# Kernel optimization log

Hardware: AMD Instinct MI355X
Metric: run time of the kernel (lower is better)

## Reference

```python
import jax, jax.numpy as jnp
import numpy as np

BN_EPS = 1e-5
N_LAYERS = 3


def _mlp_bn(h, w1, b1, g, beta, w2, b2):
    # Linear -> BatchNorm1d (batch stats, training-mode math) -> ReLU -> Linear
    h = h @ w1 + b1
    mu = jnp.mean(h, axis=0)
    var = jnp.var(h, axis=0)
    h = (h - mu) * jax.lax.rsqrt(var + BN_EPS) * g + beta
    h = jax.nn.relu(h)
    return h @ w2 + b2


def setup_inputs() -> dict:
    key = jax.random.key(0)
    ks = jax.random.split(key, 20)
    N, E, XD, ED, H, C, G = 50000, 640000, 64, 16, 128, 10, 512
    L = N_LAYERS
    s = lambda fan: 1.0 / np.sqrt(fan)
    inp = {
        "x": jax.random.normal(ks[0], (N, XD), jnp.float32),
        "edge_attr": jax.random.normal(ks[1], (E, ED), jnp.float32),
        "node_w": jax.random.uniform(ks[2], (XD, H), jnp.float32, -s(XD), s(XD)),
        "node_b": jnp.zeros((H,), jnp.float32),
        "edge_w": jax.random.uniform(ks[3], (ED, H), jnp.float32, -s(ED), s(ED)),
        "edge_b": jnp.zeros((H,), jnp.float32),
        "lin1_w": jax.random.uniform(ks[4], (L, H, H), jnp.float32, -s(H), s(H)),
        "lin1_b": jnp.zeros((L, H), jnp.float32),
        "bn_g": jnp.ones((L, H), jnp.float32),
        "bn_b": jnp.zeros((L, H), jnp.float32),
        "lin2_w": jax.random.uniform(ks[5], (L, H, H), jnp.float32, -s(H), s(H)),
        "lin2_b": jnp.zeros((L, H), jnp.float32),
        "fc_w": jax.random.uniform(ks[6], (H, C), jnp.float32, -s(H), s(H)),
        "fc_b": jnp.zeros((C,), jnp.float32),
        "edge_index": jax.random.randint(ks[7], (2, E), 0, N, jnp.int64),
        "batch": jnp.sort(jax.random.randint(ks[8], (N,), 0, G, jnp.int64)),
        "num_graphs": G,
    }
    return inp


def reference(x, edge_attr, node_w, node_b, edge_w, edge_b, lin1_w, lin1_b,
              bn_g, bn_b, lin2_w, lin2_b, fc_w, fc_b, edge_index, batch, num_graphs):
    N = x.shape[0]
    src, dst = edge_index[0], edge_index[1]
    h = x @ node_w + node_b                      # [N, H] node encoder
    e = edge_attr @ edge_w + edge_b              # [E, H] edge encoder
    for i in range(N_LAYERS):
        # GINEConv: msg = relu(h[src] + e); aggr = segment_sum at dst; out = MLP(h + aggr) (eps=0)
        msg = jax.nn.relu(h[src] + e)            # [E, H]
        aggr = jax.ops.segment_sum(msg, dst, num_segments=N)
        h = _mlp_bn(h + aggr, lin1_w[i], lin1_b[i], bn_g[i], bn_b[i], lin2_w[i], lin2_b[i])
        h = jax.nn.relu(h)                       # dropout p=0 -> identity
    pooled = jax.ops.segment_sum(h, batch, num_segments=num_graphs)  # global_add_pool
    return pooled @ fc_w + fc_b
```

## Files before the change

### kernel.cpp

```cpp
#include <hip/hip_runtime.h>

#define H   128

typedef __attribute__((ext_vector_type(8))) short short8;
typedef __attribute__((ext_vector_type(4))) float f32x4;

__device__ __forceinline__ unsigned int bfr(float f) {
  unsigned int u = __float_as_uint(f);
  return (u + 0x7fffu + ((u >> 16) & 1u)) >> 16;
}
__device__ __forceinline__ float bf_lo(unsigned int d) {
  return __uint_as_float(d << 16);
}
__device__ __forceinline__ float bf_hi(unsigned int d) {
  return __uint_as_float(d & 0xffff0000u);
}

__global__ __launch_bounds__(128) void node_enc(const float* __restrict__ x,
    const float* __restrict__ w, const float* __restrict__ b,
    unsigned int* __restrict__ h2, int N) {
  int row = blockIdx.x;
  if (row >= N) return;
  int j = threadIdx.x;
  __shared__ float xs[64];
  if (j < 64) xs[j] = x[(size_t)row * 64 + j];
  __syncthreads();
  float acc = b[j];
#pragma unroll
  for (int k = 0; k < 64; ++k) acc = fmaf(xs[k], w[k * H + j], acc);
  float part = __shfl_down(acc, 1, 64);
  if ((j & 1) == 0) {
    unsigned int d = bfr(acc) | (bfr(part) << 16);
    h2[(size_t)row * 64 + (j >> 1)] = d;
  }
}

__global__ __launch_bounds__(256) void count_deg(const int* __restrict__ dst,
    int* __restrict__ cnt, int E) {
  int e = blockIdx.x * 256 + threadIdx.x;
  if (e < E) atomicAdd(&cnt[dst[e]], 1);
}

__global__ __launch_bounds__(256) void block_sum(const int* __restrict__ cnt,
    int* __restrict__ bsum, int N) {
  int t = threadIdx.x;
  int i = blockIdx.x * 256 + t;
  int v = (i < N) ? cnt[i] : 0;
#pragma unroll
  for (int o = 32; o > 0; o >>= 1) v += __shfl_down(v, o, 64);
  __shared__ int wt[4];
  if ((t & 63) == 0) wt[t >> 6] = v;
  __syncthreads();
  if (t == 0) bsum[blockIdx.x] = wt[0] + wt[1] + wt[2] + wt[3];
}

__global__ __launch_bounds__(1024) void scan_bsum(const int* __restrict__ bsum,
    int* __restrict__ bbase, int nb) {
  __shared__ int s[1024];
  int t = threadIdx.x;
  int v = (t < nb) ? bsum[t] : 0;
  s[t] = v;
  __syncthreads();
  for (int o = 1; o < 1024; o <<= 1) {
    int u = (t >= o) ? s[t - o] : 0;
    __syncthreads();
    s[t] += u;
    __syncthreads();
  }
  if (t < nb) bbase[t] = s[t] - v;
}

__global__ __launch_bounds__(256) void scan_pass(const int* __restrict__ cnt,
    const int* __restrict__ bbase, int* __restrict__ off,
    int* __restrict__ cursor, int N) {
  int t = threadIdx.x;
  int i = blockIdx.x * 256 + t;
  int v = (i < N) ? cnt[i] : 0;
  int lane = t & 63;
  int incl = v;
#pragma unroll
  for (int o = 1; o < 64; o <<= 1) {
    int u = __shfl_up(incl, o, 64);
    if (lane >= o) incl += u;
  }
  __shared__ int wtot[4];
  int w = t >> 6;
  if (lane == 63) wtot[w] = incl;
  __syncthreads();
  if (t == 0) {
    int run = 0;
#pragma unroll
    for (int k = 0; k < 4; ++k) { int tmp = wtot[k]; wtot[k] = run; run += tmp; }
  }
  __syncthreads();
  int excl = incl - v + wtot[w] + bbase[blockIdx.x];
  if (i < N) { off[i] = excl; cursor[i] = excl; }
  if (i == N - 1) off[N] = excl + v;
}

__global__ __launch_bounds__(256) void scatter_csr(const int* __restrict__ src,
    const int* __restrict__ dst, int* __restrict__ cursor,
    int* __restrict__ perm, int* __restrict__ src_perm, int E) {
  int e = blockIdx.x * 256 + threadIdx.x;
  if (e < E) {
    int pos = atomicAdd(&cursor[dst[e]], 1);
    perm[pos] = e;
    src_perm[pos] = src[e];
  }
}

__global__ __launch_bounds__(256) void wpack(const float* __restrict__ w1,
    const float* __restrict__ w2, unsigned short* __restrict__ wp, int L) {
  int idx = blockIdx.x * 256 + threadIdx.x;
  int total = L * 2 * 16384;
  if (idx >= total) return;
  int j    = idx & 7;
  int lane = (idx >> 3) & 63;
  int ct   = (idx >> 9) & 7;
  int kt   = (idx >> 12) & 3;
  int mat  = idx >> 14;
  int l = mat >> 1, which = mat & 1;
  const float* w = (which == 0 ? w1 : w2) + (size_t)l * H * H;
  int k = kt * 32 + (lane >> 4) * 8 + j;
  int n = ct * 16 + (lane & 15);
  wp[idx] = (unsigned short)bfr(w[k * H + n]);
}

__global__ __launch_bounds__(256) void aggr_csr(const float* __restrict__ ea,
    const float* __restrict__ ew, const float* __restrict__ eb,
    const int* __restrict__ perm, const int* __restrict__ src_perm,
    const int* __restrict__ off, const unsigned int* __restrict__ h2,
    unsigned int* __restrict__ zb, int N) {
  int wid = threadIdx.x >> 6, lane = threadIdx.x & 63;
  int n = blockIdx.x * 4 + wid;
  if (n >= N) return;
  int beg = off[n], end = off[n + 1];
  int c = lane * 2;
  float2 wc[16];
#pragma unroll
  for (int k = 0; k < 16; ++k) wc[k] = *(const float2*)&ew[k * H + c];
  float2 bias = *(const float2*)&eb[c];
  float ax = 0.f, ay = 0.f;
  int i = beg;
  for (; i + 2 <= end; i += 2) {
    int e0 = __builtin_amdgcn_readfirstlane(perm[i]);
    int e1 = __builtin_amdgcn_readfirstlane(perm[i + 1]);
    int s0 = __builtin_amdgcn_readfirstlane(src_perm[i]);
    int s1 = __builtin_amdgcn_readfirstlane(src_perm[i + 1]);
    unsigned int hv0 = h2[(size_t)s0 * 64 + lane];
    unsigned int hv1 = h2[(size_t)s1 * 64 + lane];
    const float* a0 = ea + (size_t)e0 * 16;
    const float* a1 = ea + (size_t)e1 * 16;
    float x0 = bias.x, y0 = bias.y, x1 = bias.x, y1 = bias.y;
#pragma unroll
    for (int k = 0; k < 16; ++k) {
      float a0k = a0[k], a1k = a1[k];
      x0 = fmaf(a0k, wc[k].x, x0);
      y0 = fmaf(a0k, wc[k].y, y0);
      x1 = fmaf(a1k, wc[k].x, x1);
      y1 = fmaf(a1k, wc[k].y, y1);
    }
    ax += fmaxf(x0 + bf_lo(hv0), 0.f) + fmaxf(x1 + bf_lo(hv1), 0.f);
    ay += fmaxf(y0 + bf_hi(hv0), 0.f) + fmaxf(y1 + bf_hi(hv1), 0.f);
  }
  if (i < end) {
    int e0 = __builtin_amdgcn_readfirstlane(perm[i]);
    int s0 = __builtin_amdgcn_readfirstlane(src_perm[i]);
    unsigned int hv0 = h2[(size_t)s0 * 64 + lane];
    const float* a0 = ea + (size_t)e0 * 16;
    float x0 = bias.x, y0 = bias.y;
#pragma unroll
    for (int k = 0; k < 16; ++k) {
      float a0k = a0[k];
      x0 = fmaf(a0k, wc[k].x, x0);
      y0 = fmaf(a0k, wc[k].y, y0);
    }
    ax += fmaxf(x0 + bf_lo(hv0), 0.f);
    ay += fmaxf(y0 + bf_hi(hv0), 0.f);
  }
  unsigned int hn = h2[(size_t)n * 64 + lane];
  float zx = bf_lo(hn) + ax, zy = bf_hi(hn) + ay;
  zb[(size_t)n * 64 + lane] = bfr(zx) | (bfr(zy) << 16);
}

__global__ __launch_bounds__(256) void mlp1m(const unsigned short* __restrict__ zb,
    const unsigned short* __restrict__ wp, const float* __restrict__ b1,
    float* __restrict__ tout, float* __restrict__ sum,
    float* __restrict__ sumsq, int N) {
  int tid = threadIdx.x;
  int wave = tid >> 6, lane = tid & 63;
  int q = lane >> 4, m = lane & 15;
  int r0 = blockIdx.x * 64 + wave * 16;
  f32x4 acc[8];
#pragma unroll
  for (int ct = 0; ct < 8; ++ct) acc[ct] = (f32x4){0.f, 0.f, 0.f, 0.f};
#pragma unroll
  for (int kt = 0; kt < 4; ++kt) {
    short8 a = *(const short8*)(zb + (size_t)(r0 + m) * H + kt * 32 + q * 8);
#pragma unroll
    for (int ct = 0; ct < 8; ++ct) {
      short8 b = *(const short8*)(wp + ((size_t)(kt * 8 + ct) * 64 + lane) * 8);
      acc[ct] = __builtin_amdgcn_mfma_f32_16x16x32_bf16(a, b, acc[ct], 0, 0, 0);
    }
  }
  __shared__ float red[2][H][16];
  int wq = wave * 4 + q;
#pragma unroll
  for (int ct = 0; ct < 8; ++ct) {
    int col = ct * 16 + m;
    float bias = b1[col];
    float s1 = 0.f, s2 = 0.f;
#pragma unroll
    for (int r = 0; r < 4; ++r) {
      int gr = r0 + q * 4 + r;
      float v = acc[ct][r] + bias;
      if (gr < N) {
        tout[(size_t)gr * H + col] = v;
        s1 += v;
        s2 += v * v;
      }
    }
    red[0][col][wq] = s1;
    red[1][col][wq] = s2;
  }
  __syncthreads();
  if (tid < H) {
    float a = 0.f, b = 0.f;
#pragma unroll
    for (int g = 0; g < 16; ++g) {
      a += red[0][tid][g];
      b += red[1][tid][g];
    }
    atomicAdd(&sum[tid], a);
    atomicAdd(&sumsq[tid], b);
  }
}

__global__ void bn_finalize(const float* __restrict__ sum,
    const float* __restrict__ sumsq, const float* __restrict__ g,
    const float* __restrict__ beta, float* __restrict__ scale,
    float* __restrict__ shift, float invN) {
  int j = threadIdx.x;
  float mu = sum[j] * invN;
  float var = sumsq[j] * invN - mu * mu;
  float inv = rsqrtf(var + 1e-5f);
  float sc = g[j] * inv;
  scale[j] = sc;
  shift[j] = beta[j] - mu * sc;
}

__global__ __launch_bounds__(256) void mlp2m(const float* __restrict__ tin,
    const float* __restrict__ scale, const float* __restrict__ shift,
    const unsigned short* __restrict__ wp, const float* __restrict__ b2,
    unsigned short* __restrict__ hout, int N,
    const int* __restrict__ batch, float* __restrict__ pooled) {
  int tid = threadIdx.x;
  int wave = tid >> 6, lane = tid & 63;
  int q = lane >> 4, m = lane & 15;
  int r0 = blockIdx.x * 64 + wave * 16;
  f32x4 acc[8];
#pragma unroll
  for (int ct = 0; ct < 8; ++ct) acc[ct] = (f32x4){0.f, 0.f, 0.f, 0.f};
#pragma unroll
  for (int kt = 0; kt < 4; ++kt) {
    int col0 = kt * 32 + q * 8;
    f32x4 t0 = *(const f32x4*)(tin + (size_t)(r0 + m) * H + col0);
    f32x4 t1 = *(const f32x4*)(tin + (size_t)(r0 + m) * H + col0 + 4);
    f32x4 sc0 = *(const f32x4*)(scale + col0);
    f32x4 sc1 = *(const f32x4*)(scale + col0 + 4);
    f32x4 sh0 = *(const f32x4*)(shift + col0);
    f32x4 sh1 = *(const f32x4*)(shift + col0 + 4);
    short8 a;
#pragma unroll
    for (int j = 0; j < 4; ++j) {
      float v = fmaxf(fmaf(t0[j], sc0[j], sh0[j]), 0.f);
      a[j] = (short)bfr(v);
    }
#pragma unroll
    for (int j = 0; j < 4; ++j) {
      float v = fmaxf(fmaf(t1[j], sc1[j], sh1[j]), 0.f);
      a[4 + j] = (short)bfr(v);
    }
#pragma unroll
    for (int ct = 0; ct < 8; ++ct) {
      short8 b = *(const short8*)(wp + ((size_t)(kt * 8 + ct) * 64 + lane) * 8);
      acc[ct] = __builtin_amdgcn_mfma_f32_16x16x32_bf16(a, b, acc[ct], 0, 0, 0);
    }
  }
#pragma unroll
  for (int ct = 0; ct < 8; ++ct) {
    float bias = b2[ct * 16 + m];
#pragma unroll
    for (int r = 0; r < 4; ++r) acc[ct][r] = fmaxf(acc[ct][r] + bias, 0.f);
  }
  if (hout != nullptr) {
#pragma unroll
    for (int r = 0; r < 4; ++r) {
      int gr = r0 + q * 4 + r;
      if (gr < N) {
#pragma unroll
        for (int ct = 0; ct < 8; ++ct)
          hout[(size_t)gr * H + ct * 16 + m] = (unsigned short)bfr(acc[ct][r]);
      }
    }
  }
  if (pooled != nullptr) {
    int bprev = -1;
    float pa[8];
#pragma unroll
    for (int ct = 0; ct < 8; ++ct) pa[ct] = 0.f;
    for (int r = 0; r < 4; ++r) {
      int gr = r0 + q * 4 + r;
      if (gr >= N) break;
      int bb = batch[gr];
      if (bb != bprev && bprev >= 0) {
#pragma unroll
        for (int ct = 0; ct < 8; ++ct) {
          atomicAdd(&pooled[(size_t)bprev * H + ct * 16 + m], pa[ct]);
          pa[ct] = 0.f;
        }
      }
      bprev = bb;
#pragma unroll
      for (int ct = 0; ct < 8; ++ct) pa[ct] += acc[ct][r];
    }
    if (bprev >= 0) {
#pragma unroll
      for (int ct = 0; ct < 8; ++ct)
        atomicAdd(&pooled[(size_t)bprev * H + ct * 16 + m], pa[ct]);
    }
  }
}

__global__ __launch_bounds__(128) void fc_kernel(const float* __restrict__ pooled,
    const float* __restrict__ w, const float* __restrict__ b,
    float* __restrict__ out, int C) {
  int g = blockIdx.x;
  int j = threadIdx.x;
  __shared__ float p[H];
  p[j] = pooled[(size_t)g * H + j];
  __syncthreads();
  if (j < C) {
    float acc = b[j];
#pragma unroll 4
    for (int k = 0; k < H; ++k) acc = fmaf(p[k], w[k * C + j], acc);
    out[(size_t)g * C + j] = acc;
  }
}

extern "C" void kernel_launch(void* const* d_in, const int* in_sizes, int n_in,
                              void* d_out, int out_size, void* d_ws, size_t ws_size,
                              hipStream_t stream) {
  const float* x         = (const float*)d_in[0];
  const float* edge_attr = (const float*)d_in[1];
  const float* node_w    = (const float*)d_in[2];
  const float* node_b    = (const float*)d_in[3];
  const float* edge_w    = (const float*)d_in[4];
  const float* edge_b    = (const float*)d_in[5];
  const float* lin1_w    = (const float*)d_in[6];
  const float* lin1_b    = (const float*)d_in[7];
  const float* bn_g      = (const float*)d_in[8];
  const float* bn_b      = (const float*)d_in[9];
  const float* lin2_w    = (const float*)d_in[10];
  const float* lin2_b    = (const float*)d_in[11];
  const float* fc_w      = (const float*)d_in[12];
  const float* fc_b      = (const float*)d_in[13];
  const int*   edge_index= (const int*)d_in[14];
  const int*   batch     = (const int*)d_in[15];

  int N = in_sizes[0] / 64;
  int E = in_sizes[1] / 16;
  int C = in_sizes[13];
  int G = out_size / C;

  const int* src = edge_index;
  const int* dst = edge_index + E;

  int mblk = (N + 63) / 64;
  int Npad = mblk * 64;

  float* t      = (float*)d_ws;
  float* pooled = t + (size_t)Npad * H;
  float* sums   = pooled + (size_t)G * H;
  float* sumsq  = sums + H;
  float* scale  = sumsq + H;
  float* shift  = scale + H;
  unsigned int* h2 = (unsigned int*)(shift + H);
  unsigned int* zb = h2 + (size_t)Npad * 64;
  unsigned short* wp = (unsigned short*)(zb + (size_t)Npad * 64);
  int* cnt      = (int*)(wp + 6 * 16384);
  int* off      = cnt + N;
  int* cursor   = off + N + 1;
  int* src_perm = cursor + N;
  int* perm     = src_perm + E;
  int* bsum     = perm + E;
  int* bbase    = bsum + 1024;

  int nb = (N + 255) / 256;

  hipMemsetAsync(cnt, 0, (size_t)N * sizeof(int), stream);
  count_deg<<<(E + 255) / 256, 256, 0, stream>>>(dst, cnt, E);
  block_sum<<<nb, 256, 0, stream>>>(cnt, bsum, N);
  scan_bsum<<<1, 1024, 0, stream>>>(bsum, bbase, nb);
  scan_pass<<<nb, 256, 0, stream>>>(cnt, bbase, off, cursor, N);
  scatter_csr<<<(E + 255) / 256, 256, 0, stream>>>(src, dst, cursor, perm, src_perm, E);
  wpack<<<(6 * 16384 + 255) / 256, 256, 0, stream>>>(lin1_w, lin2_w, wp, 3);

  node_enc<<<N, 128, 0, stream>>>(x, node_w, node_b, h2, N);

  int ablk = (N + 3) / 4;
  for (int l = 0; l < 3; ++l) {
    hipMemsetAsync(sums, 0, 2 * H * sizeof(float), stream);
    aggr_csr<<<ablk, 256, 0, stream>>>(edge_attr, edge_w, edge_b, perm,
                                       src_perm, off, h2, zb, N);
    mlp1m<<<mblk, 256, 0, stream>>>((const unsigned short*)zb,
                                    wp + (size_t)(l * 2 + 0) * 16384,
                                    lin1_b + (size_t)l * H, t, sums, sumsq, N);
    bn_finalize<<<1, H, 0, stream>>>(sums, sumsq, bn_g + (size_t)l * H,
                                     bn_b + (size_t)l * H, scale, shift, 1.0f / N);
    bool last = (l == 2);
    if (last) hipMemsetAsync(pooled, 0, (size_t)G * H * sizeof(float), stream);
    mlp2m<<<mblk, 256, 0, stream>>>(t, scale, shift,
                                    wp + (size_t)(l * 2 + 1) * 16384,
                                    lin2_b + (size_t)l * H,
                                    last ? nullptr : (unsigned short*)h2, N,
                                    batch, last ? pooled : nullptr);
  }

  fc_kernel<<<G, 128, 0, stream>>>(pooled, fc_w, fc_b, (float*)d_out, C);
}
```

Before: 629.8 us.

## Balance edge aggregation with fixed-size edge chunks and boundary atomics

Replaces the per-node CSR aggregation, where each wave handled one destination node, with an edge-balanced scheme. Each wave now takes a fixed-size chunk of dst-sorted edges and flushes partial sums with float atomics into an fp32 z buffer whenever the destination changes. The h+aggr addition and bf16 conversion move into mlp1m. bn_finalize is folded into the prologue of mlp2m, and the BN stat buffers are zeroed once up front. The intent is to remove load imbalance from variable node degrees and drop launches, at the cost of a per-layer memset of an N×H fp32 buffer, more atomics, and doubled z traffic in fp32.

After: 646.7 us. 2.7% more time.

```diff
diff --git a/kernel.cpp b/kernel.cpp
--- a/kernel.cpp
+++ b/kernel.cpp
@@ -100,12 +100,15 @@
 
 __global__ __launch_bounds__(256) void scatter_csr(const int* __restrict__ src,
     const int* __restrict__ dst, int* __restrict__ cursor,
-    int* __restrict__ perm, int* __restrict__ src_perm, int E) {
+    int* __restrict__ perm, int* __restrict__ src_perm,
+    int* __restrict__ dst_perm, int E) {
   int e = blockIdx.x * 256 + threadIdx.x;
   if (e < E) {
-    int pos = atomicAdd(&cursor[dst[e]], 1);
+    int d = dst[e];
+    int pos = atomicAdd(&cursor[d], 1);
     perm[pos] = e;
     src_perm[pos] = src[e];
+    dst_perm[pos] = d;
   }
 }
 
@@ -126,27 +129,31 @@
   wp[idx] = (unsigned short)bfr(w[k * H + n]);
 }
 
-__global__ __launch_bounds__(256) void aggr_csr(const float* __restrict__ ea,
+__global__ __launch_bounds__(256) void aggr_chunk(const float* __restrict__ ea,
     const float* __restrict__ ew, const float* __restrict__ eb,
     const int* __restrict__ perm, const int* __restrict__ src_perm,
-    const int* __restrict__ off, const unsigned int* __restrict__ h2,
-    unsigned int* __restrict__ zb, int N) {
-  int wid = threadIdx.x >> 6, lane = threadIdx.x & 63;
-  int n = blockIdx.x * 4 + wid;
-  if (n >= N) return;
-  int beg = off[n], end = off[n + 1];
+    const int* __restrict__ dst_perm, const unsigned int* __restrict__ h2,
+    float* __restrict__ z, int E, int CH) {
+  int wv = blockIdx.x * 4 + (threadIdx.x >> 6);
+  int lane = threadIdx.x & 63;
+  int i0 = wv * CH;
+  int i1 = min(E, i0 + CH);
+  if (i0 >= i1) return;
   int c = lane * 2;
   float2 wc[16];
 #pragma unroll
   for (int k = 0; k < 16; ++k) wc[k] = *(const float2*)&ew[k * H + c];
   float2 bias = *(const float2*)&eb[c];
+  int cur = __builtin_amdgcn_readfirstlane(dst_perm[i0]);
   float ax = 0.f, ay = 0.f;
-  int i = beg;
-  for (; i + 2 <= end; i += 2) {
+  int i = i0;
+  for (; i + 2 <= i1; i += 2) {
     int e0 = __builtin_amdgcn_readfirstlane(perm[i]);
     int e1 = __builtin_amdgcn_readfirstlane(perm[i + 1]);
     int s0 = __builtin_amdgcn_readfirstlane(src_perm[i]);
     int s1 = __builtin_amdgcn_readfirstlane(src_perm[i + 1]);
+    int d0 = __builtin_amdgcn_readfirstlane(dst_perm[i]);
+    int d1 = __builtin_amdgcn_readfirstlane(dst_perm[i + 1]);
     unsigned int hv0 = h2[(size_t)s0 * 64 + lane];
     unsigned int hv1 = h2[(size_t)s1 * 64 + lane];
     const float* a0 = ea + (size_t)e0 * 16;
@@ -160,12 +167,27 @@
       x1 = fmaf(a1k, wc[k].x, x1);
       y1 = fmaf(a1k, wc[k].y, y1);
     }
-    ax += fmaxf(x0 + bf_lo(hv0), 0.f) + fmaxf(x1 + bf_lo(hv1), 0.f);
-    ay += fmaxf(y0 + bf_hi(hv0), 0.f) + fmaxf(y1 + bf_hi(hv1), 0.f);
-  }
-  if (i < end) {
+    if (d0 != cur) {
+      atomicAdd(&z[(size_t)cur * H + c], ax);
+      atomicAdd(&z[(size_t)cur * H + c + 1], ay);
+      ax = ay = 0.f;
+      cur = d0;
+    }
+    ax += fmaxf(x0 + bf_lo(hv0), 0.f);
+    ay += fmaxf(y0 + bf_hi(hv0), 0.f);
+    if (d1 != cur) {
+      atomicAdd(&z[(size_t)cur * H + c], ax);
+      atomicAdd(&z[(size_t)cur * H + c + 1], ay);
+      ax = ay = 0.f;
+      cur = d1;
+    }
+    ax += fmaxf(x1 + bf_lo(hv1), 0.f);
+    ay += fmaxf(y1 + bf_hi(hv1), 0.f);
+  }
+  if (i < i1) {
     int e0 = __builtin_amdgcn_readfirstlane(perm[i]);
     int s0 = __builtin_amdgcn_readfirstlane(src_perm[i]);
+    int d0 = __builtin_amdgcn_readfirstlane(dst_perm[i]);
     unsigned int hv0 = h2[(size_t)s0 * 64 + lane];
     const float* a0 = ea + (size_t)e0 * 16;
     float x0 = bias.x, y0 = bias.y;
@@ -175,28 +197,46 @@
       x0 = fmaf(a0k, wc[k].x, x0);
       y0 = fmaf(a0k, wc[k].y, y0);
     }
+    if (d0 != cur) {
+      atomicAdd(&z[(size_t)cur * H + c], ax);
+      atomicAdd(&z[(size_t)cur * H + c + 1], ay);
+      ax = ay = 0.f;
+      cur = d0;
+    }
     ax += fmaxf(x0 + bf_lo(hv0), 0.f);
     ay += fmaxf(y0 + bf_hi(hv0), 0.f);
   }
-  unsigned int hn = h2[(size_t)n * 64 + lane];
-  float zx = bf_lo(hn) + ax, zy = bf_hi(hn) + ay;
-  zb[(size_t)n * 64 + lane] = bfr(zx) | (bfr(zy) << 16);
-}
-
-__global__ __launch_bounds__(256) void mlp1m(const unsigned short* __restrict__ zb,
-    const unsigned short* __restrict__ wp, const float* __restrict__ b1,
-    float* __restrict__ tout, float* __restrict__ sum,
-    float* __restrict__ sumsq, int N) {
+  atomicAdd(&z[(size_t)cur * H + c], ax);
+  atomicAdd(&z[(size_t)cur * H + c + 1], ay);
+}
+
+__global__ __launch_bounds__(256) void mlp1m(const float* __restrict__ z,
+    const unsigned int* __restrict__ h2, const unsigned short* __restrict__ wp,
+    const float* __restrict__ b1, float* __restrict__ tout,
+    float* __restrict__ sum, float* __restrict__ sumsq, int N) {
   int tid = threadIdx.x;
   int wave = tid >> 6, lane = tid & 63;
   int q = lane >> 4, m = lane & 15;
   int r0 = blockIdx.x * 64 + wave * 16;
+  int row = r0 + m;
   f32x4 acc[8];
 #pragma unroll
   for (int ct = 0; ct < 8; ++ct) acc[ct] = (f32x4){0.f, 0.f, 0.f, 0.f};
 #pragma unroll
   for (int kt = 0; kt < 4; ++kt) {
-    short8 a = *(const short8*)(zb + (size_t)(r0 + m) * H + kt * 32 + q * 8);
+    int c0 = kt * 32 + q * 8;
+    f32x4 z0 = *(const f32x4*)(z + (size_t)row * H + c0);
+    f32x4 z1 = *(const f32x4*)(z + (size_t)row * H + c0 + 4);
+    uint4 hh = *(const uint4*)(h2 + (size_t)row * 64 + (c0 >> 1));
+    short8 a;
+    a[0] = (short)bfr(z0[0] + bf_lo(hh.x));
+    a[1] = (short)bfr(z0[1] + bf_hi(hh.x));
+    a[2] = (short)bfr(z0[2] + bf_lo(hh.y));
+    a[3] = (short)bfr(z0[3] + bf_hi(hh.y));
+    a[4] = (short)bfr(z1[0] + bf_lo(hh.z));
+    a[5] = (short)bfr(z1[1] + bf_hi(hh.z));
+    a[6] = (short)bfr(z1[2] + bf_lo(hh.w));
+    a[7] = (short)bfr(z1[3] + bf_hi(hh.w));
 #pragma unroll
     for (int ct = 0; ct < 8; ++ct) {
       short8 b = *(const short8*)(wp + ((size_t)(kt * 8 + ct) * 64 + lane) * 8);
@@ -236,49 +276,44 @@
   }
 }
 
-__global__ void bn_finalize(const float* __restrict__ sum,
-    const float* __restrict__ sumsq, const float* __restrict__ g,
-    const float* __restrict__ beta, float* __restrict__ scale,
-    float* __restrict__ shift, float invN) {
-  int j = threadIdx.x;
-  float mu = sum[j] * invN;
-  float var = sumsq[j] * invN - mu * mu;
-  float inv = rsqrtf(var + 1e-5f);
-  float sc = g[j] * inv;
-  scale[j] = sc;
-  shift[j] = beta[j] - mu * sc;
-}
-
 __global__ __launch_bounds__(256) void mlp2m(const float* __restrict__ tin,
-    const float* __restrict__ scale, const float* __restrict__ shift,
+    const float* __restrict__ sums, const float* __restrict__ sumsqs,
+    const float* __restrict__ bng, const float* __restrict__ bnb,
     const unsigned short* __restrict__ wp, const float* __restrict__ b2,
-    unsigned short* __restrict__ hout, int N,
+    unsigned short* __restrict__ hout, int N, float invN,
     const int* __restrict__ batch, float* __restrict__ pooled) {
   int tid = threadIdx.x;
+  __shared__ float scs[H], shs[H];
+  if (tid < H) {
+    float mu = sums[tid] * invN;
+    float var = sumsqs[tid] * invN - mu * mu;
+    float inv = rsqrtf(var + 1e-5f);
+    float sc = bng[tid] * inv;
+    scs[tid] = sc;
+    shs[tid] = bnb[tid] - mu * sc;
+  }
+  __syncthreads();
   int wave = tid >> 6, lane = tid & 63;
   int q = lane >> 4, m = lane & 15;
   int r0 = blockIdx.x * 64 + wave * 16;
+  int row = r0 + m;
   f32x4 acc[8];
 #pragma unroll
   for (int ct = 0; ct < 8; ++ct) acc[ct] = (f32x4){0.f, 0.f, 0.f, 0.f};
 #pragma unroll
   for (int kt = 0; kt < 4; ++kt) {
-    int col0 = kt * 32 + q * 8;
-    f32x4 t0 = *(const f32x4*)(tin + (size_t)(r0 + m) * H + col0);
-    f32x4 t1 = *(const f32x4*)(tin + (size_t)(r0 + m) * H + col0 + 4);
-    f32x4 sc0 = *(const f32x4*)(scale + col0);
-    f32x4 sc1 = *(const f32x4*)(scale + col0 + 4);
-    f32x4 sh0 = *(const f32x4*)(shift + col0);
-    f32x4 sh1 = *(const f32x4*)(shift + col0 + 4);
+    int c0 = kt * 32 + q * 8;
+    f32x4 t0 = *(const f32x4*)(tin + (size_t)row * H + c0);
+    f32x4 t1 = *(const f32x4*)(tin + (size_t)row * H + c0 + 4);
     short8 a;
 #pragma unroll
     for (int j = 0; j < 4; ++j) {
-      float v = fmaxf(fmaf(t0[j], sc0[j], sh0[j]), 0.f);
+      float v = fmaxf(fmaf(t0[j], scs[c0 + j], shs[c0 + j]), 0.f);
       a[j] = (short)bfr(v);
     }
 #pragma unroll
     for (int j = 0; j < 4; ++j) {
-      float v = fmaxf(fmaf(t1[j], sc1[j], sh1[j]), 0.f);
+      float v = fmaxf(fmaf(t1[j], scs[c0 + 4 + j], shs[c0 + 4 + j]), 0.f);
       a[4 + j] = (short)bfr(v);
     }
 #pragma unroll
@@ -380,19 +415,17 @@
   int Npad = mblk * 64;
 
   float* t      = (float*)d_ws;
-  float* pooled = t + (size_t)Npad * H;
-  float* sums   = pooled + (size_t)G * H;
-  float* sumsq  = sums + H;
-  float* scale  = sumsq + H;
-  float* shift  = scale + H;
-  unsigned int* h2 = (unsigned int*)(shift + H);
-  unsigned int* zb = h2 + (size_t)Npad * 64;
-  unsigned short* wp = (unsigned short*)(zb + (size_t)Npad * 64);
+  float* z      = t + (size_t)Npad * H;
+  float* pooled = z + (size_t)Npad * H;
+  float* sumsA  = pooled + (size_t)G * H;
+  unsigned int* h2 = (unsigned int*)(sumsA + 3 * 256);
+  unsigned short* wp = (unsigned short*)(h2 + (size_t)Npad * 64);
   int* cnt      = (int*)(wp + 6 * 16384);
   int* off      = cnt + N;
   int* cursor   = off + N + 1;
   int* src_perm = cursor + N;
-  int* perm     = src_perm + E;
+  int* dst_perm = src_perm + E;
+  int* perm     = dst_perm + E;
   int* bsum     = perm + E;
   int* bbase    = bsum + 1024;
 
@@ -403,28 +436,32 @@
   block_sum<<<nb, 256, 0, stream>>>(cnt, bsum, N);
   scan_bsum<<<1, 1024, 0, stream>>>(bsum, bbase, nb);
   scan_pass<<<nb, 256, 0, stream>>>(cnt, bbase, off, cursor, N);
-  scatter_csr<<<(E + 255) / 256, 256, 0, stream>>>(src, dst, cursor, perm, src_perm, E);
+  scatter_csr<<<(E + 255) / 256, 256, 0, stream>>>(src, dst, cursor, perm,
+                                                   src_perm, dst_perm, E);
   wpack<<<(6 * 16384 + 255) / 256, 256, 0, stream>>>(lin1_w, lin2_w, wp, 3);
+  hipMemsetAsync(sumsA, 0, 3 * 256 * sizeof(float), stream);
 
   node_enc<<<N, 128, 0, stream>>>(x, node_w, node_b, h2, N);
 
-  int ablk = (N + 3) / 4;
+  const int NWAVE = 8192;
+  int CH = (E + NWAVE - 1) / NWAVE;
+  int ablk = ( (E + CH - 1) / CH + 3 ) / 4;
+
   for (int l = 0; l < 3; ++l) {
-    hipMemsetAsync(sums, 0, 2 * H * sizeof(float), stream);
-    aggr_csr<<<ablk, 256, 0, stream>>>(edge_attr, edge_w, edge_b, perm,
-                                       src_perm, off, h2, zb, N);
-    mlp1m<<<mblk, 256, 0, stream>>>((const unsigned short*)zb,
-                                    wp + (size_t)(l * 2 + 0) * 16384,
-                                    lin1_b + (size_t)l * H, t, sums, sumsq, N);
-    bn_finalize<<<1, H, 0, stream>>>(sums, sumsq, bn_g + (size_t)l * H,
-                                     bn_b + (size_t)l * H, scale, shift, 1.0f / N);
+    hipMemsetAsync(z, 0, (size_t)N * H * sizeof(float), stream);
+    aggr_chunk<<<ablk, 256, 0, stream>>>(edge_attr, edge_w, edge_b, perm,
+                                         src_perm, dst_perm, h2, z, E, CH);
+    mlp1m<<<mblk, 256, 0, stream>>>(z, h2, wp + (size_t)(l * 2 + 0) * 16384,
+                                    lin1_b + (size_t)l * H, t,
+                                    sumsA + l * 256, sumsA + l * 256 + 128, N);
     bool last = (l == 2);
     if (last) hipMemsetAsync(pooled, 0, (size_t)G * H * sizeof(float), stream);
-    mlp2m<<<mblk, 256, 0, stream>>>(t, scale, shift,
+    mlp2m<<<mblk, 256, 0, stream>>>(t, sumsA + l * 256, sumsA + l * 256 + 128,
+                                    bn_g + (size_t)l * H, bn_b + (size_t)l * H,
                                     wp + (size_t)(l * 2 + 1) * 16384,
                                     lin2_b + (size_t)l * H,
                                     last ? nullptr : (unsigned short*)h2, N,
-                                    batch, last ? pooled : nullptr);
+                                    1.0f / N, batch, last ? pooled : nullptr);
   }
 
   fc_kernel<<<G, 128, 0, stream>>>(pooled, fc_w, fc_b, (float*)d_out, C);
```

## Fuse setup kernels, pack edge/src indices, unroll aggregation by four, fold BN finalize

Applied to the files above, without the earlier changes.

Merges degree counting, node encoding and weight packing into one grid-stride prep kernel. All zero-init memsets are collapsed into a single memset, and per-layer BN sums get separate slots. bn_finalize is folded into mlp2m via shared memory. The CSR now stores edge id and source as one int2, and the aggregation loop handles four edges per iteration for more memory-level parallelism. Together these cut launch count and index loads at the cost of more registers in aggr_csr and redundant BN finalize work in every mlp2m block.

Result: slower. 670.1 us (+6.4%).

```diff
diff --git a/kernel.cpp b/kernel.cpp
--- a/kernel.cpp
+++ b/kernel.cpp
@@ -16,29 +16,40 @@
   return __uint_as_float(d & 0xffff0000u);
 }
 
-__global__ __launch_bounds__(128) void node_enc(const float* __restrict__ x,
-    const float* __restrict__ w, const float* __restrict__ b,
-    unsigned int* __restrict__ h2, int N) {
-  int row = blockIdx.x;
-  if (row >= N) return;
-  int j = threadIdx.x;
-  __shared__ float xs[64];
-  if (j < 64) xs[j] = x[(size_t)row * 64 + j];
-  __syncthreads();
-  float acc = b[j];
-#pragma unroll
-  for (int k = 0; k < 64; ++k) acc = fmaf(xs[k], w[k * H + j], acc);
-  float part = __shfl_down(acc, 1, 64);
-  if ((j & 1) == 0) {
-    unsigned int d = bfr(acc) | (bfr(part) << 16);
-    h2[(size_t)row * 64 + (j >> 1)] = d;
-  }
-}
-
-__global__ __launch_bounds__(256) void count_deg(const int* __restrict__ dst,
-    int* __restrict__ cnt, int E) {
-  int e = blockIdx.x * 256 + threadIdx.x;
-  if (e < E) atomicAdd(&cnt[dst[e]], 1);
+__global__ __launch_bounds__(256) void prep(const int* __restrict__ dst,
+    int* __restrict__ cnt, int E, const float* __restrict__ x,
+    const float* __restrict__ node_w, const float* __restrict__ node_b,
+    unsigned int* __restrict__ h2, int N, const float* __restrict__ lin1_w,
+    const float* __restrict__ lin2_w, unsigned short* __restrict__ wp) {
+  int gtid = blockIdx.x * 256 + threadIdx.x;
+  int GT = gridDim.x * 256;
+  for (int e = gtid; e < E; e += GT) atomicAdd(&cnt[dst[e]], 1);
+  int lane = threadIdx.x & 63;
+  int wg = blockIdx.x * 4 + (threadIdx.x >> 6);
+  int NW = gridDim.x * 4;
+  int c = lane * 2;
+  float b0 = node_b[c], b1 = node_b[c + 1];
+  for (int row = wg; row < N; row += NW) {
+    const float* xr = x + (size_t)row * 64;
+    float a0 = b0, a1 = b1;
+#pragma unroll 8
+    for (int k = 0; k < 64; ++k) {
+      float xk = xr[k];
+      float2 wv = *(const float2*)&node_w[k * H + c];
+      a0 = fmaf(xk, wv.x, a0);
+      a1 = fmaf(xk, wv.y, a1);
+    }
+    h2[(size_t)row * 64 + lane] = bfr(a0) | (bfr(a1) << 16);
+  }
+  for (int idx = gtid; idx < 6 * 16384; idx += GT) {
+    int j = idx & 7, ln = (idx >> 3) & 63, ct = (idx >> 9) & 7;
+    int kt = (idx >> 12) & 3, mat = idx >> 14;
+    int l = mat >> 1, which = mat & 1;
+    const float* w = (which == 0 ? lin1_w : lin2_w) + (size_t)l * H * H;
+    int k = kt * 32 + (ln >> 4) * 8 + j;
+    int n = ct * 16 + (ln & 15);
+    wp[idx] = (unsigned short)bfr(w[k * H + n]);
+  }
 }
 
 __global__ __launch_bounds__(256) void block_sum(const int* __restrict__ cnt,
@@ -100,37 +111,19 @@
 
 __global__ __launch_bounds__(256) void scatter_csr(const int* __restrict__ src,
     const int* __restrict__ dst, int* __restrict__ cursor,
-    int* __restrict__ perm, int* __restrict__ src_perm, int E) {
+    int2* __restrict__ es, int E) {
   int e = blockIdx.x * 256 + threadIdx.x;
   if (e < E) {
     int pos = atomicAdd(&cursor[dst[e]], 1);
-    perm[pos] = e;
-    src_perm[pos] = src[e];
-  }
-}
-
-__global__ __launch_bounds__(256) void wpack(const float* __restrict__ w1,
-    const float* __restrict__ w2, unsigned short* __restrict__ wp, int L) {
-  int idx = blockIdx.x * 256 + threadIdx.x;
-  int total = L * 2 * 16384;
-  if (idx >= total) return;
-  int j    = idx & 7;
-  int lane = (idx >> 3) & 63;
-  int ct   = (idx >> 9) & 7;
-  int kt   = (idx >> 12) & 3;
-  int mat  = idx >> 14;
-  int l = mat >> 1, which = mat & 1;
-  const float* w = (which == 0 ? w1 : w2) + (size_t)l * H * H;
-  int k = kt * 32 + (lane >> 4) * 8 + j;
-  int n = ct * 16 + (lane & 15);
-  wp[idx] = (unsigned short)bfr(w[k * H + n]);
+    es[pos] = make_int2(e, src[e]);
+  }
 }
 
 __global__ __launch_bounds__(256) void aggr_csr(const float* __restrict__ ea,
     const float* __restrict__ ew, const float* __restrict__ eb,
-    const int* __restrict__ perm, const int* __restrict__ src_perm,
-    const int* __restrict__ off, const unsigned int* __restrict__ h2,
-    unsigned int* __restrict__ zb, int N) {
+    const int2* __restrict__ es, const int* __restrict__ off,
+    const unsigned int* __restrict__ h2, unsigned int* __restrict__ zb,
+    int N) {
   int wid = threadIdx.x >> 6, lane = threadIdx.x & 63;
   int n = blockIdx.x * 4 + wid;
   if (n >= N) return;
@@ -142,30 +135,44 @@
   float2 bias = *(const float2*)&eb[c];
   float ax = 0.f, ay = 0.f;
   int i = beg;
-  for (; i + 2 <= end; i += 2) {
-    int e0 = __builtin_amdgcn_readfirstlane(perm[i]);
-    int e1 = __builtin_amdgcn_readfirstlane(perm[i + 1]);
-    int s0 = __builtin_amdgcn_readfirstlane(src_perm[i]);
-    int s1 = __builtin_amdgcn_readfirstlane(src_perm[i + 1]);
+  for (; i + 4 <= end; i += 4) {
+    int2 p0 = es[i], p1 = es[i + 1], p2 = es[i + 2], p3 = es[i + 3];
+    int e0 = __builtin_amdgcn_readfirstlane(p0.x);
+    int s0 = __builtin_amdgcn_readfirstlane(p0.y);
+    int e1 = __builtin_amdgcn_readfirstlane(p1.x);
+    int s1 = __builtin_amdgcn_readfirstlane(p1.y);
+    int e2 = __builtin_amdgcn_readfirstlane(p2.x);
+    int s2 = __builtin_amdgcn_readfirstlane(p2.y);
+    int e3 = __builtin_amdgcn_readfirstlane(p3.x);
+    int s3 = __builtin_amdgcn_readfirstlane(p3.y);
     unsigned int hv0 = h2[(size_t)s0 * 64 + lane];
     unsigned int hv1 = h2[(size_t)s1 * 64 + lane];
+    unsigned int hv2 = h2[(size_t)s2 * 64 + lane];
+    unsigned int hv3 = h2[(size_t)s3 * 64 + lane];
     const float* a0 = ea + (size_t)e0 * 16;
     const float* a1 = ea + (size_t)e1 * 16;
+    const float* a2 = ea + (size_t)e2 * 16;
+    const float* a3 = ea + (size_t)e3 * 16;
     float x0 = bias.x, y0 = bias.y, x1 = bias.x, y1 = bias.y;
+    float x2 = bias.x, y2 = bias.y, x3 = bias.x, y3 = bias.y;
 #pragma unroll
     for (int k = 0; k < 16; ++k) {
-      float a0k = a0[k], a1k = a1[k];
-      x0 = fmaf(a0k, wc[k].x, x0);
-      y0 = fmaf(a0k, wc[k].y, y0);
-      x1 = fmaf(a1k, wc[k].x, x1);
-      y1 = fmaf(a1k, wc[k].y, y1);
-    }
-    ax += fmaxf(x0 + bf_lo(hv0), 0.f) + fmaxf(x1 + bf_lo(hv1), 0.f);
-    ay += fmaxf(y0 + bf_hi(hv0), 0.f) + fmaxf(y1 + bf_hi(hv1), 0.f);
-  }
-  if (i < end) {
-    int e0 = __builtin_amdgcn_readfirstlane(perm[i]);
-    int s0 = __builtin_amdgcn_readfirstlane(src_perm[i]);
+      float a0k = a0[k], a1k = a1[k], a2k = a2[k], a3k = a3[k];
+      float2 w = wc[k];
+      x0 = fmaf(a0k, w.x, x0); y0 = fmaf(a0k, w.y, y0);
+      x1 = fmaf(a1k, w.x, x1); y1 = fmaf(a1k, w.y, y1);
+      x2 = fmaf(a2k, w.x, x2); y2 = fmaf(a2k, w.y, y2);
+      x3 = fmaf(a3k, w.x, x3); y3 = fmaf(a3k, w.y, y3);
+    }
+    ax += fmaxf(x0 + bf_lo(hv0), 0.f) + fmaxf(x1 + bf_lo(hv1), 0.f) +
+          fmaxf(x2 + bf_lo(hv2), 0.f) + fmaxf(x3 + bf_lo(hv3), 0.f);
+    ay += fmaxf(y0 + bf_hi(hv0), 0.f) + fmaxf(y1 + bf_hi(hv1), 0.f) +
+          fmaxf(y2 + bf_hi(hv2), 0.f) + fmaxf(y3 + bf_hi(hv3), 0.f);
+  }
+  for (; i < end; ++i) {
+    int2 p0 = es[i];
+    int e0 = __builtin_amdgcn_readfirstlane(p0.x);
+    int s0 = __builtin_amdgcn_readfirstlane(p0.y);
     unsigned int hv0 = h2[(size_t)s0 * 64 + lane];
     const float* a0 = ea + (size_t)e0 * 16;
     float x0 = bias.x, y0 = bias.y;
@@ -179,8 +186,8 @@
     ay += fmaxf(y0 + bf_hi(hv0), 0.f);
   }
   unsigned int hn = h2[(size_t)n * 64 + lane];
-  float zx = bf_lo(hn) + ax, zy = bf_hi(hn) + ay;
-  zb[(size_t)n * 64 + lane] = bfr(zx) | (bfr(zy) << 16);
+  zb[(size_t)n * 64 + lane] =
+      bfr(bf_lo(hn) + ax) | (bfr(bf_hi(hn) + ay) << 16);
 }
 
 __global__ __launch_bounds__(256) void mlp1m(const unsigned short* __restrict__ zb,
@@ -236,49 +243,44 @@
   }
 }
 
-__global__ void bn_finalize(const float* __restrict__ sum,
-    const float* __restrict__ sumsq, const float* __restrict__ g,
-    const float* __restrict__ beta, float* __restrict__ scale,
-    float* __restrict__ shift, float invN) {
-  int j = threadIdx.x;
-  float mu = sum[j] * invN;
-  float var = sumsq[j] * invN - mu * mu;
-  float inv = rsqrtf(var + 1e-5f);
-  float sc = g[j] * inv;
-  scale[j] = sc;
-  shift[j] = beta[j] - mu * sc;
-}
-
 __global__ __launch_bounds__(256) void mlp2m(const float* __restrict__ tin,
-    const float* __restrict__ scale, const float* __restrict__ shift,
+    const float* __restrict__ sums, const float* __restrict__ sumsqs,
+    const float* __restrict__ bng, const float* __restrict__ bnb,
     const unsigned short* __restrict__ wp, const float* __restrict__ b2,
-    unsigned short* __restrict__ hout, int N,
+    unsigned short* __restrict__ hout, int N, float invN,
     const int* __restrict__ batch, float* __restrict__ pooled) {
   int tid = threadIdx.x;
+  __shared__ float scs[H], shs[H];
+  if (tid < H) {
+    float mu = sums[tid] * invN;
+    float var = sumsqs[tid] * invN - mu * mu;
+    float inv = rsqrtf(var + 1e-5f);
+    float sc = bng[tid] * inv;
+    scs[tid] = sc;
+    shs[tid] = bnb[tid] - mu * sc;
+  }
+  __syncthreads();
   int wave = tid >> 6, lane = tid & 63;
   int q = lane >> 4, m = lane & 15;
   int r0 = blockIdx.x * 64 + wave * 16;
+  int row = r0 + m;
   f32x4 acc[8];
 #pragma unroll
   for (int ct = 0; ct < 8; ++ct) acc[ct] = (f32x4){0.f, 0.f, 0.f, 0.f};
 #pragma unroll
   for (int kt = 0; kt < 4; ++kt) {
-    int col0 = kt * 32 + q * 8;
-    f32x4 t0 = *(const f32x4*)(tin + (size_t)(r0 + m) * H + col0);
-    f32x4 t1 = *(const f32x4*)(tin + (size_t)(r0 + m) * H + col0 + 4);
-    f32x4 sc0 = *(const f32x4*)(scale + col0);
-    f32x4 sc1 = *(const f32x4*)(scale + col0 + 4);
-    f32x4 sh0 = *(const f32x4*)(shift + col0);
-    f32x4 sh1 = *(const f32x4*)(shift + col0 + 4);
+    int c0 = kt * 32 + q * 8;
+    f32x4 t0 = *(const f32x4*)(tin + (size_t)row * H + c0);
+    f32x4 t1 = *(const f32x4*)(tin + (size_t)row * H + c0 + 4);
     short8 a;
 #pragma unroll
     for (int j = 0; j < 4; ++j) {
-      float v = fmaxf(fmaf(t0[j], sc0[j], sh0[j]), 0.f);
+      float v = fmaxf(fmaf(t0[j], scs[c0 + j], shs[c0 + j]), 0.f);
       a[j] = (short)bfr(v);
     }
 #pragma unroll
     for (int j = 0; j < 4; ++j) {
-      float v = fmaxf(fmaf(t1[j], sc1[j], sh1[j]), 0.f);
+      float v = fmaxf(fmaf(t1[j], scs[c0 + 4 + j], shs[c0 + 4 + j]), 0.f);
       a[4 + j] = (short)bfr(v);
     }
 #pragma unroll
@@ -378,53 +380,45 @@
 
   int mblk = (N + 63) / 64;
   int Npad = mblk * 64;
+  int nb = (N + 255) / 256;
 
   float* t      = (float*)d_ws;
   float* pooled = t + (size_t)Npad * H;
-  float* sums   = pooled + (size_t)G * H;
-  float* sumsq  = sums + H;
-  float* scale  = sumsq + H;
-  float* shift  = scale + H;
-  unsigned int* h2 = (unsigned int*)(shift + H);
+  float* sumsA  = pooled + (size_t)G * H;
+  int*   cnt    = (int*)(sumsA + 3 * 256);
+  size_t zbytes = ((size_t)G * H + 3 * 256 + N) * 4;
+  int*   off    = cnt + N;
+  int*   cursor = off + N + 2;
+  int2*  es     = (int2*)(cursor + N);
+  unsigned int* h2 = (unsigned int*)(es + E);
   unsigned int* zb = h2 + (size_t)Npad * 64;
   unsigned short* wp = (unsigned short*)(zb + (size_t)Npad * 64);
-  int* cnt      = (int*)(wp + 6 * 16384);
-  int* off      = cnt + N;
-  int* cursor   = off + N + 1;
-  int* src_perm = cursor + N;
-  int* perm     = src_perm + E;
-  int* bsum     = perm + E;
-  int* bbase    = bsum + 1024;
-
-  int nb = (N + 255) / 256;
-
-  hipMemsetAsync(cnt, 0, (size_t)N * sizeof(int), stream);
-  count_deg<<<(E + 255) / 256, 256, 0, stream>>>(dst, cnt, E);
+  int* bsum  = (int*)(wp + 6 * 16384);
+  int* bbase = bsum + 1024;
+
+  hipMemsetAsync(pooled, 0, zbytes, stream);
+  prep<<<1024, 256, 0, stream>>>(dst, cnt, E, x, node_w, node_b, h2, N,
+                                 lin1_w, lin2_w, wp);
   block_sum<<<nb, 256, 0, stream>>>(cnt, bsum, N);
   scan_bsum<<<1, 1024, 0, stream>>>(bsum, bbase, nb);
   scan_pass<<<nb, 256, 0, stream>>>(cnt, bbase, off, cursor, N);
-  scatter_csr<<<(E + 255) / 256, 256, 0, stream>>>(src, dst, cursor, perm, src_perm, E);
-  wpack<<<(6 * 16384 + 255) / 256, 256, 0, stream>>>(lin1_w, lin2_w, wp, 3);
-
-  node_enc<<<N, 128, 0, stream>>>(x, node_w, node_b, h2, N);
+  scatter_csr<<<(E + 255) / 256, 256, 0, stream>>>(src, dst, cursor, es, E);
 
   int ablk = (N + 3) / 4;
   for (int l = 0; l < 3; ++l) {
-    hipMemsetAsync(sums, 0, 2 * H * sizeof(float), stream);
-    aggr_csr<<<ablk, 256, 0, stream>>>(edge_attr, edge_w, edge_b, perm,
-                                       src_perm, off, h2, zb, N);
+    aggr_csr<<<ablk, 256, 0, stream>>>(edge_attr, edge_w, edge_b, es, off,
+                                       h2, zb, N);
     mlp1m<<<mblk, 256, 0, stream>>>((const unsigned short*)zb,
-                                    wp + (size_t)(l * 2 + 0) * 16384,
-                                    lin1_b + (size_t)l * H, t, sums, sumsq, N);
-    bn_finalize<<<1, H, 0, stream>>>(sums, sumsq, bn_g + (size_t)l * H,
-                                     bn_b + (size_t)l * H, scale, shift, 1.0f / N);
+                                    wp + (size_t)(l * 2) * 16384,
+                                    lin1_b + (size_t)l * H, t,
+                                    sumsA + l * 256, sumsA + l * 256 + 128, N);
     bool last = (l == 2);
-    if (last) hipMemsetAsync(pooled, 0, (size_t)G * H * sizeof(float), stream);
-    mlp2m<<<mblk, 256, 0, stream>>>(t, scale, shift,
+    mlp2m<<<mblk, 256, 0, stream>>>(t, sumsA + l * 256, sumsA + l * 256 + 128,
+                                    bn_g + (size_t)l * H, bn_b + (size_t)l * H,
                                     wp + (size_t)(l * 2 + 1) * 16384,
                                     lin2_b + (size_t)l * H,
                                     last ? nullptr : (unsigned short*)h2, N,
-                                    batch, last ? pooled : nullptr);
+                                    1.0f / N, batch, last ? pooled : nullptr);
   }
 
   fc_kernel<<<G, 128, 0, stream>>>(pooled, fc_w, fc_b, (float*)d_out, C);
```
